# Kernel optimization log

Hardware: AMD Instinct MI355X
Metric: run time of the kernel (lower is better)

## Reference

```python
import jax, jax.numpy as jnp
import numpy as np

B, N_SITES, N_BONDS = 16, 2048, 65536
SITE_LEN, BOND_LEN, STATE_LEN = 64, 64, 64
H1, H2 = 256, 256


def setup_inputs() -> dict:
    key = jax.random.key(0)
    ks = jax.random.split(key, 10)
    d_in = SITE_LEN + BOND_LEN + STATE_LEN
    s = lambda fan_in: 1.0 / np.sqrt(fan_in)
    return {
        "sites": jax.random.normal(ks[0], (B, N_SITES, SITE_LEN), jnp.float32),
        "bonds": jax.random.normal(ks[1], (B, N_BONDS, BOND_LEN), jnp.float32),
        "states": jax.random.normal(ks[2], (B, STATE_LEN), jnp.float32),
        "indices1": jax.random.randint(ks[3], (N_BONDS,), 0, N_SITES),
        "W1": jax.random.uniform(ks[4], (d_in, H1), jnp.float32, -s(d_in), s(d_in)),
        "b1": jnp.zeros((H1,), jnp.float32),
        "W2": jax.random.uniform(ks[5], (H1, H2), jnp.float32, -s(H1), s(H1)),
        "b2": jnp.zeros((H2,), jnp.float32),
        "W3": jax.random.uniform(ks[6], (H2, SITE_LEN), jnp.float32, -s(H2), s(H2)),
        "b3": jnp.zeros((SITE_LEN,), jnp.float32),
    }


def reference(sites, bonds, states, indices1, W1, b1, W2, b2, W3, b3):
    n_sites = sites.shape[1]
    # scatter_mean over the bond axis (dim=1). indices shared across batch, so
    # put bonds axis leading and use a single segment_sum: [n_bonds, B, bond_len]
    seg_sum = jax.ops.segment_sum(jnp.swapaxes(bonds, 0, 1), indices1,
                                  num_segments=n_sites)          # [n_sites, B, bond_len]
    counts = jax.ops.segment_sum(jnp.ones((bonds.shape[1],), bonds.dtype),
                                 indices1, num_segments=n_sites)  # [n_sites]
    denom = jnp.maximum(counts, 1.0)[:, None, None]
    bonds_pool = jnp.swapaxes(seg_sum / denom, 0, 1)              # [B, n_sites, bond_len]
    states1 = jnp.broadcast_to(states[:, None, :],
                               (sites.shape[0], n_sites, states.shape[-1]))
    v = jnp.concatenate([bonds_pool, sites, states1], axis=2)
    h = jax.nn.relu(v @ W1 + b1)
    h = jax.nn.relu(h @ W2 + b2)
    return jax.nn.relu(h @ W3 + b3)
```

## Files before the change

kernel.cpp:

```cpp
#include <hip/hip_runtime.h>
#include <cstdint>
#include <cstddef>

typedef _Float16 f16;
typedef f16 f16x8 __attribute__((ext_vector_type(8)));
typedef f16 f16x4 __attribute__((ext_vector_type(4)));
typedef float f32x4 __attribute__((ext_vector_type(4)));

constexpr int NS = 2048;
constexpr int NB = 65536;

__global__ void pack_kernel(const float* __restrict__ W1, const float* __restrict__ W2,
                            const float* __restrict__ W3, f16* __restrict__ pw1,
                            f16* __restrict__ pw2, f16* __restrict__ pw3) {
    int t = blockIdx.x * 256 + threadIdx.x;
    int tt = t >> 6, l = t & 63;
    const float* W; f16* dst; int N, tloc, kt, nt;
    if (tt < 96)       { W = W1; dst = pw1; N = 256; tloc = tt;       kt = tloc >> 4; nt = tloc & 15; }
    else if (tt < 224) { W = W2; dst = pw2; N = 256; tloc = tt - 96;  kt = tloc >> 4; nt = tloc & 15; }
    else               { W = W3; dst = pw3; N = 64;  tloc = tt - 224; kt = tloc >> 2; nt = tloc & 3;  }
    int kbase = kt * 32 + (l >> 4) * 8;
    int n = nt * 16 + (l & 15);
    f16x8 o;
    #pragma unroll
    for (int j = 0; j < 8; ++j) o[j] = (f16)W[(size_t)(kbase + j) * N + n];
    *reinterpret_cast<f16x8*>(&dst[(size_t)(tloc * 64 + l) * 8]) = o;
}

__global__ __launch_bounds__(256, 4) void fused_kernel(
    const float* __restrict__ bonds, const float* __restrict__ sites, const float* __restrict__ states,
    const int* __restrict__ idx,
    const float* __restrict__ b1, const float* __restrict__ b2, const float* __restrict__ b3,
    const f16x8* __restrict__ pw1, const f16x8* __restrict__ pw2, const f16x8* __restrict__ pw3,
    float* __restrict__ out) {
    constexpr int STR = 280;
    __shared__ f16 bufA[32 * STR];
    __shared__ f16 bufB[32 * STR];
    __shared__ int qcnt[32];
    int t = threadIdx.x;
    int w = t >> 6, lane = t & 63;
    int arow = lane & 15, ag = lane >> 4;
    int blk = blockIdx.x;
    int b = blk >> 6;
    int s0 = (blk & 63) * 32;
    int m0 = b * NS + s0;

    int* queue = reinterpret_cast<int*>(bufB);

    if (t < 32) qcnt[t] = 0;
    __syncthreads();

    {
        const int4* idx4 = reinterpret_cast<const int4*>(idx);
        #pragma unroll 4
        for (int k = 0; k < 64; ++k) {
            int i4 = k * 256 + t;
            int4 v = idx4[i4];
            int base_i = i4 * 4;
            #pragma unroll
            for (int e = 0; e < 4; ++e) {
                int s = (&v.x)[e];
                unsigned d = (unsigned)(s - s0);
                if (d < 32u) {
                    int pos = atomicAdd(&qcnt[d], 1);
                    queue[d * 128 + pos] = base_i + e;
                }
            }
        }
    }
    {
        #pragma unroll
        for (int p = 0; p < 2; ++p) {
            int i = p * 256 + t;
            int row = i >> 4, c4 = i & 15;
            f32x4 v = *reinterpret_cast<const f32x4*>(sites + (size_t)(m0 + row) * 64 + c4 * 4);
            f16x4 h = { (f16)v[0], (f16)v[1], (f16)v[2], (f16)v[3] };
            *reinterpret_cast<f16x4*>(&bufA[row * STR + 64 + c4 * 4]) = h;
        }
        f32x4 v = *reinterpret_cast<const f32x4*>(states + (size_t)b * 64 + (t & 15) * 4);
        f16x4 h = { (f16)v[0], (f16)v[1], (f16)v[2], (f16)v[3] };
        #pragma unroll
        for (int p = 0; p < 2; ++p) {
            int row = p * 16 + (t >> 4), c4 = t & 15;
            *reinterpret_cast<f16x4*>(&bufA[row * STR + 128 + c4 * 4]) = h;
        }
    }
    __syncthreads();

    {
        int slot = t >> 4, f4 = t & 15;
        const f32x4* base = reinterpret_cast<const f32x4*>(bonds) + (size_t)b * NB * 16;
        #pragma unroll
        for (int sg = 0; sg < 2; ++sg) {
            int srow = sg * 16 + slot;
            int cnt = qcnt[srow];
            const int* qrow = queue + srow * 128;
            f32x4 acc = {0.f, 0.f, 0.f, 0.f};
            int i = 0;
            for (; i + 8 <= cnt; i += 8) {
                int id[8];
                #pragma unroll
                for (int u = 0; u < 8; ++u) id[u] = qrow[i + u];
                f32x4 v[8];
                #pragma unroll
                for (int u = 0; u < 8; ++u) v[u] = base[(size_t)id[u] * 16 + f4];
                #pragma unroll
                for (int u = 0; u < 8; ++u) acc += v[u];
            }
            for (; i + 4 <= cnt; i += 4) {
                int id0 = qrow[i + 0], id1 = qrow[i + 1], id2 = qrow[i + 2], id3 = qrow[i + 3];
                f32x4 v0 = base[(size_t)id0 * 16 + f4];
                f32x4 v1 = base[(size_t)id1 * 16 + f4];
                f32x4 v2 = base[(size_t)id2 * 16 + f4];
                f32x4 v3 = base[(size_t)id3 * 16 + f4];
                acc += v0; acc += v1; acc += v2; acc += v3;
            }
            for (; i < cnt; ++i) acc += base[(size_t)qrow[i] * 16 + f4];
            float inv = 1.0f / (float)(cnt > 1 ? cnt : 1);
            acc *= inv;
            f16x4 h = { (f16)acc[0], (f16)acc[1], (f16)acc[2], (f16)acc[3] };
            *reinterpret_cast<f16x4*>(&bufA[srow * STR + f4 * 4]) = h;
        }
    }
    __syncthreads();

    {
        f32x4 acc[2][4];
        #pragma unroll
        for (int ni = 0; ni < 4; ++ni) {
            float bv = b1[w * 64 + ni * 16 + arow];
            acc[0][ni] = f32x4{bv, bv, bv, bv};
            acc[1][ni] = f32x4{bv, bv, bv, bv};
        }
        #pragma unroll
        for (int kt = 0; kt < 6; ++kt) {
            f16x8 af[2], bfr[4];
            #pragma unroll
            for (int mi = 0; mi < 2; ++mi)
                af[mi] = *reinterpret_cast<const f16x8*>(&bufA[(mi * 16 + arow) * STR + kt * 32 + ag * 8]);
            #pragma unroll
            for (int ni = 0; ni < 4; ++ni) bfr[ni] = pw1[(kt * 16 + w * 4 + ni) * 64 + lane];
            #pragma unroll
            for (int mi = 0; mi < 2; ++mi)
                #pragma unroll
                for (int ni = 0; ni < 4; ++ni)
                    acc[mi][ni] = __builtin_amdgcn_mfma_f32_16x16x32_f16(af[mi], bfr[ni], acc[mi][ni], 0, 0, 0);
        }
        __syncthreads();
        #pragma unroll
        for (int mi = 0; mi < 2; ++mi)
            #pragma unroll
            for (int ni = 0; ni < 4; ++ni)
                #pragma unroll
                for (int j = 0; j < 4; ++j) {
                    float x = acc[mi][ni][j]; x = x > 0.f ? x : 0.f;
                    bufB[(mi * 16 + ag * 4 + j) * STR + w * 64 + ni * 16 + arow] = (f16)x;
                }
    }
    __syncthreads();

    {
        f32x4 acc[2][4];
        #pragma unroll
        for (int ni = 0; ni < 4; ++ni) {
            float bv = b2[w * 64 + ni * 16 + arow];
            acc[0][ni] = f32x4{bv, bv, bv, bv};
            acc[1][ni] = f32x4{bv, bv, bv, bv};
        }
        #pragma unroll
        for (int kt = 0; kt < 8; ++kt) {
            f16x8 af[2], bfr[4];
            #pragma unroll
            for (int mi = 0; mi < 2; ++mi)
                af[mi] = *reinterpret_cast<const f16x8*>(&bufB[(mi * 16 + arow) * STR + kt * 32 + ag * 8]);
            #pragma unroll
            for (int ni = 0; ni < 4; ++ni) bfr[ni] = pw2[(kt * 16 + w * 4 + ni) * 64 + lane];
            #pragma unroll
            for (int mi = 0; mi < 2; ++mi)
                #pragma unroll
                for (int ni = 0; ni < 4; ++ni)
                    acc[mi][ni] = __builtin_amdgcn_mfma_f32_16x16x32_f16(af[mi], bfr[ni], acc[mi][ni], 0, 0, 0);
        }
        __syncthreads();
        #pragma unroll
        for (int mi = 0; mi < 2; ++mi)
            #pragma unroll
            for (int ni = 0; ni < 4; ++ni)
                #pragma unroll
                for (int j = 0; j < 4; ++j) {
                    float x = acc[mi][ni][j]; x = x > 0.f ? x : 0.f;
                    bufA[(mi * 16 + ag * 4 + j) * STR + w * 64 + ni * 16 + arow] = (f16)x;
                }
    }
    __syncthreads();

    {
        f32x4 acc[2];
        float bv = b3[w * 16 + arow];
        acc[0] = f32x4{bv, bv, bv, bv};
        acc[1] = f32x4{bv, bv, bv, bv};
        #pragma unroll
        for (int kt = 0; kt < 8; ++kt) {
            f16x8 bfr = pw3[(kt * 4 + w) * 64 + lane];
            #pragma unroll
            for (int mi = 0; mi < 2; ++mi) {
                f16x8 af = *reinterpret_cast<const f16x8*>(&bufA[(mi * 16 + arow) * STR + kt * 32 + ag * 8]);
                acc[mi] = __builtin_amdgcn_mfma_f32_16x16x32_f16(af, bfr, acc[mi], 0, 0, 0);
            }
        }
        #pragma unroll
        for (int mi = 0; mi < 2; ++mi)
            #pragma unroll
            for (int j = 0; j < 4; ++j) {
                float x = acc[mi][j]; x = x > 0.f ? x : 0.f;
                out[(size_t)(m0 + mi * 16 + ag * 4 + j) * 64 + w * 16 + arow] = x;
            }
    }
}

extern "C" void kernel_launch(void* const* d_in, const int* in_sizes, int n_in,
                              void* d_out, int out_size, void* d_ws, size_t ws_size,
                              hipStream_t stream) {
    (void)in_sizes; (void)n_in; (void)out_size; (void)ws_size;
    const float* sites  = (const float*)d_in[0];
    const float* bonds  = (const float*)d_in[1];
    const float* states = (const float*)d_in[2];
    const int*   idx    = (const int*)d_in[3];
    const float* W1 = (const float*)d_in[4];
    const float* b1 = (const float*)d_in[5];
    const float* W2 = (const float*)d_in[6];
    const float* b2 = (const float*)d_in[7];
    const float* W3 = (const float*)d_in[8];
    const float* b3 = (const float*)d_in[9];
    float* out = (float*)d_out;

    char* ws = (char*)d_ws;
    f16* pw1 = (f16*)ws;
    f16* pw2 = pw1 + 96 * 512;
    f16* pw3 = pw2 + 128 * 512;

    pack_kernel<<<64, 256, 0, stream>>>(W1, W2, W3, pw1, pw2, pw3);
    fused_kernel<<<1024, 256, 0, stream>>>(bonds, sites, states, idx,
                                           b1, b2, b3,
                                           (const f16x8*)pw1, (const f16x8*)pw2, (const f16x8*)pw3, out);
}
```

Before: 85.65 us.

## Build CSR bucket of bond indices once in prep kernel instead of per block

Replaces the per-block scan of all 65536 indices (each of 1024 blocks filtering its 32 sites via LDS atomics) with a single prep block that counts, prefix-scans and buckets bond indices into a global CSR layout, fused with weight packing. The main kernel then reads counts, offsets and its bucket directly, removing a large redundant index pass and several barriers. The gather loop is also unrolled to 16 with a masked tail. The cost is that one 1024-thread block does the whole bucketing serially before the main kernel can start, and the bucketed order within a site is nondeterministic.

New measurement: 105.7 us. +23.4%, slower.

```diff
diff --git a/kernel.cpp b/kernel.cpp
--- a/kernel.cpp
+++ b/kernel.cpp
@@ -10,33 +10,77 @@
 constexpr int NS = 2048;
 constexpr int NB = 65536;
 
-__global__ void pack_kernel(const float* __restrict__ W1, const float* __restrict__ W2,
-                            const float* __restrict__ W3, f16* __restrict__ pw1,
-                            f16* __restrict__ pw2, f16* __restrict__ pw3) {
-    int t = blockIdx.x * 256 + threadIdx.x;
-    int tt = t >> 6, l = t & 63;
-    const float* W; f16* dst; int N, tloc, kt, nt;
-    if (tt < 96)       { W = W1; dst = pw1; N = 256; tloc = tt;       kt = tloc >> 4; nt = tloc & 15; }
-    else if (tt < 224) { W = W2; dst = pw2; N = 256; tloc = tt - 96;  kt = tloc >> 4; nt = tloc & 15; }
-    else               { W = W3; dst = pw3; N = 64;  tloc = tt - 224; kt = tloc >> 2; nt = tloc & 3;  }
-    int kbase = kt * 32 + (l >> 4) * 8;
-    int n = nt * 16 + (l & 15);
-    f16x8 o;
-    #pragma unroll
-    for (int j = 0; j < 8; ++j) o[j] = (f16)W[(size_t)(kbase + j) * N + n];
-    *reinterpret_cast<f16x8*>(&dst[(size_t)(tloc * 64 + l) * 8]) = o;
+__global__ __launch_bounds__(1024) void prep_kernel(
+    const float* __restrict__ W1, const float* __restrict__ W2, const float* __restrict__ W3,
+    const int* __restrict__ idx,
+    f16* __restrict__ pw1, f16* __restrict__ pw2, f16* __restrict__ pw3,
+    int* __restrict__ counts, int* __restrict__ offsets, int* __restrict__ bucket) {
+    __shared__ int cs[2048];
+    __shared__ int wsum[16];
+    if (blockIdx.x < 16) {
+        int t = blockIdx.x * 1024 + threadIdx.x;
+        int tt = t >> 6, l = t & 63;
+        const float* W; f16* dst; int N, tloc, kt, nt;
+        if (tt < 96)       { W = W1; dst = pw1; N = 256; tloc = tt;       kt = tloc >> 4; nt = tloc & 15; }
+        else if (tt < 224) { W = W2; dst = pw2; N = 256; tloc = tt - 96;  kt = tloc >> 4; nt = tloc & 15; }
+        else               { W = W3; dst = pw3; N = 64;  tloc = tt - 224; kt = tloc >> 2; nt = tloc & 3;  }
+        int kbase = kt * 32 + (l >> 4) * 8;
+        int n = nt * 16 + (l & 15);
+        f16x8 o;
+        #pragma unroll
+        for (int j = 0; j < 8; ++j) o[j] = (f16)W[(size_t)(kbase + j) * N + n];
+        *reinterpret_cast<f16x8*>(&dst[(size_t)(tloc * 64 + l) * 8]) = o;
+    } else {
+        int tid = threadIdx.x;
+        cs[tid] = 0; cs[tid + 1024] = 0;
+        __syncthreads();
+        const int4* idx4 = reinterpret_cast<const int4*>(idx);
+        #pragma unroll 4
+        for (int k = 0; k < 16; ++k) {
+            int4 v = idx4[k * 1024 + tid];
+            atomicAdd(&cs[v.x], 1); atomicAdd(&cs[v.y], 1);
+            atomicAdd(&cs[v.z], 1); atomicAdd(&cs[v.w], 1);
+        }
+        __syncthreads();
+        int c0 = cs[2 * tid], c1 = cs[2 * tid + 1];
+        counts[2 * tid] = c0; counts[2 * tid + 1] = c1;
+        int tsum = c0 + c1;
+        int lane = tid & 63, wv = tid >> 6;
+        int incl = tsum;
+        #pragma unroll
+        for (int d = 1; d < 64; d <<= 1) { int x = __shfl_up(incl, d); if (lane >= d) incl += x; }
+        if (lane == 63) wsum[wv] = incl;
+        __syncthreads();
+        int wexcl = 0;
+        #pragma unroll
+        for (int i2 = 0; i2 < 16; ++i2) wexcl += (i2 < wv) ? wsum[i2] : 0;
+        int excl = wexcl + incl - tsum;
+        offsets[2 * tid] = excl; offsets[2 * tid + 1] = excl + c0;
+        __syncthreads();
+        cs[2 * tid] = excl; cs[2 * tid + 1] = excl + c0;
+        __syncthreads();
+        #pragma unroll 4
+        for (int k = 0; k < 16; ++k) {
+            int4 v = idx4[k * 1024 + tid];
+            int i0 = (k * 1024 + tid) * 4;
+            int p;
+            p = atomicAdd(&cs[v.x], 1); bucket[p] = i0;
+            p = atomicAdd(&cs[v.y], 1); bucket[p] = i0 + 1;
+            p = atomicAdd(&cs[v.z], 1); bucket[p] = i0 + 2;
+            p = atomicAdd(&cs[v.w], 1); bucket[p] = i0 + 3;
+        }
+    }
 }
 
 __global__ __launch_bounds__(256, 4) void fused_kernel(
     const float* __restrict__ bonds, const float* __restrict__ sites, const float* __restrict__ states,
-    const int* __restrict__ idx,
+    const int* __restrict__ counts, const int* __restrict__ offsets, const int* __restrict__ bucket,
     const float* __restrict__ b1, const float* __restrict__ b2, const float* __restrict__ b3,
     const f16x8* __restrict__ pw1, const f16x8* __restrict__ pw2, const f16x8* __restrict__ pw3,
     float* __restrict__ out) {
     constexpr int STR = 280;
     __shared__ f16 bufA[32 * STR];
     __shared__ f16 bufB[32 * STR];
-    __shared__ int qcnt[32];
     int t = threadIdx.x;
     int w = t >> 6, lane = t & 63;
     int arow = lane & 15, ag = lane >> 4;
@@ -45,29 +89,6 @@
     int s0 = (blk & 63) * 32;
     int m0 = b * NS + s0;
 
-    int* queue = reinterpret_cast<int*>(bufB);
-
-    if (t < 32) qcnt[t] = 0;
-    __syncthreads();
-
-    {
-        const int4* idx4 = reinterpret_cast<const int4*>(idx);
-        #pragma unroll 4
-        for (int k = 0; k < 64; ++k) {
-            int i4 = k * 256 + t;
-            int4 v = idx4[i4];
-            int base_i = i4 * 4;
-            #pragma unroll
-            for (int e = 0; e < 4; ++e) {
-                int s = (&v.x)[e];
-                unsigned d = (unsigned)(s - s0);
-                if (d < 32u) {
-                    int pos = atomicAdd(&qcnt[d], 1);
-                    queue[d * 128 + pos] = base_i + e;
-                }
-            }
-        }
-    }
     {
         #pragma unroll
         for (int p = 0; p < 2; ++p) {
@@ -85,7 +106,6 @@
             *reinterpret_cast<f16x4*>(&bufA[row * STR + 128 + c4 * 4]) = h;
         }
     }
-    __syncthreads();
 
     {
         int slot = t >> 4, f4 = t & 15;
@@ -93,29 +113,35 @@
         #pragma unroll
         for (int sg = 0; sg < 2; ++sg) {
             int srow = sg * 16 + slot;
-            int cnt = qcnt[srow];
-            const int* qrow = queue + srow * 128;
+            int s = s0 + srow;
+            int cnt = counts[s];
+            const int* q = bucket + offsets[s];
             f32x4 acc = {0.f, 0.f, 0.f, 0.f};
             int i = 0;
+            for (; i + 16 <= cnt; i += 16) {
+                f32x4 v[16];
+                #pragma unroll
+                for (int u = 0; u < 16; ++u) v[u] = base[q[i + u] * 16 + f4];
+                #pragma unroll
+                for (int u = 0; u < 16; ++u) acc += v[u];
+            }
             for (; i + 8 <= cnt; i += 8) {
-                int id[8];
-                #pragma unroll
-                for (int u = 0; u < 8; ++u) id[u] = qrow[i + u];
                 f32x4 v[8];
                 #pragma unroll
-                for (int u = 0; u < 8; ++u) v[u] = base[(size_t)id[u] * 16 + f4];
+                for (int u = 0; u < 8; ++u) v[u] = base[q[i + u] * 16 + f4];
                 #pragma unroll
                 for (int u = 0; u < 8; ++u) acc += v[u];
             }
-            for (; i + 4 <= cnt; i += 4) {
-                int id0 = qrow[i + 0], id1 = qrow[i + 1], id2 = qrow[i + 2], id3 = qrow[i + 3];
-                f32x4 v0 = base[(size_t)id0 * 16 + f4];
-                f32x4 v1 = base[(size_t)id1 * 16 + f4];
-                f32x4 v2 = base[(size_t)id2 * 16 + f4];
-                f32x4 v3 = base[(size_t)id3 * 16 + f4];
-                acc += v0; acc += v1; acc += v2; acc += v3;
-            }
-            for (; i < cnt; ++i) acc += base[(size_t)qrow[i] * 16 + f4];
+            if (i < cnt) {
+                f32x4 v[8];
+                #pragma unroll
+                for (int u = 0; u < 8; ++u) {
+                    int j = (i + u < cnt) ? (i + u) : i;
+                    v[u] = base[q[j] * 16 + f4];
+                }
+                #pragma unroll
+                for (int u = 0; u < 8; ++u) if (i + u < cnt) acc += v[u];
+            }
             float inv = 1.0f / (float)(cnt > 1 ? cnt : 1);
             acc *= inv;
             f16x4 h = { (f16)acc[0], (f16)acc[1], (f16)acc[2], (f16)acc[3] };
@@ -146,7 +172,6 @@
                 for (int ni = 0; ni < 4; ++ni)
                     acc[mi][ni] = __builtin_amdgcn_mfma_f32_16x16x32_f16(af[mi], bfr[ni], acc[mi][ni], 0, 0, 0);
         }
-        __syncthreads();
         #pragma unroll
         for (int mi = 0; mi < 2; ++mi)
             #pragma unroll
@@ -235,12 +260,16 @@
     float* out = (float*)d_out;
 
     char* ws = (char*)d_ws;
-    f16* pw1 = (f16*)ws;
-    f16* pw2 = pw1 + 96 * 512;
-    f16* pw3 = pw2 + 128 * 512;
-
-    pack_kernel<<<64, 256, 0, stream>>>(W1, W2, W3, pw1, pw2, pw3);
-    fused_kernel<<<1024, 256, 0, stream>>>(bonds, sites, states, idx,
+    f16* pw1     = (f16*)ws;
+    f16* pw2     = pw1 + 96 * 512;
+    f16* pw3     = pw2 + 128 * 512;
+    int* counts  = (int*)(ws + 262144);
+    int* offsets = (int*)(ws + 262144 + 8192);
+    int* bucket  = (int*)(ws + 262144 + 16384);
+
+    prep_kernel<<<17, 1024, 0, stream>>>(W1, W2, W3, idx, pw1, pw2, pw3,
+                                         counts, offsets, bucket);
+    fused_kernel<<<1024, 256, 0, stream>>>(bonds, sites, states, counts, offsets, bucket,
                                            b1, b2, b3,
                                            (const f16x8*)pw1, (const f16x8*)pw2, (const f16x8*)pw3, out);
 }
```
